# Kernel optimization log

Measured on AMD Instinct MI355X. Metric: run time of the kernel, lower is better.

Reference implementation:

```python
import jax, jax.numpy as jnp
import numpy as np

D_MODEL = 2048; D_STATE = 128; D_CONV = 4; EXPAND = 2
HEADDIM = 64; NGROUPS = 1; CHUNK = 256
D_INNER = EXPAND * D_MODEL          # 4096
NHEADS = D_INNER // HEADDIM         # 64
HG = NHEADS // NGROUPS              # heads per group
CONV_DIM = D_INNER + 2 * NGROUPS * D_STATE          # 4352
D_IN_PROJ = 2 * D_INNER + 2 * NGROUPS * D_STATE + NHEADS  # 8512
BATCH = 2; SEQLEN = 2048
EPS = 1e-5


def setup_inputs() -> dict:
    ks = jax.random.split(jax.random.key(0), 8)
    u = jax.random.normal(ks[0], (BATCH, SEQLEN, D_MODEL), jnp.float32)
    in_proj_w = jax.random.normal(ks[1], (D_IN_PROJ, D_MODEL), jnp.float32) * D_MODEL ** -0.5
    conv_w = jax.random.normal(ks[2], (CONV_DIM, D_CONV), jnp.float32) * D_CONV ** -0.5
    conv_b = jax.random.normal(ks[3], (CONV_DIM,), jnp.float32) * 0.1
    # dt_bias init exactly as in the module: inv softplus of dt ~ U(log(1e-3), log(1e-1))
    dt = jnp.exp(jax.random.uniform(ks[4], (NHEADS,), jnp.float32)
                 * (np.float32(np.log(0.1)) - np.float32(np.log(0.001))) + np.float32(np.log(0.001)))
    dt = jnp.clip(dt, 1e-4, None)
    dt_bias = dt + jnp.log(-jnp.expm1(-dt))
    A_log = jnp.log(jax.random.uniform(ks[5], (NHEADS,), jnp.float32, minval=1.0, maxval=16.0))
    D_skip = jnp.ones((NHEADS,), jnp.float32)
    norm_w = jnp.ones((D_INNER,), jnp.float32)
    out_proj_w = jax.random.normal(ks[6], (D_MODEL, D_INNER), jnp.float32) * D_INNER ** -0.5
    return dict(u=u, in_proj_w=in_proj_w, conv_w=conv_w, conv_b=conv_b,
                dt_bias=dt_bias, A_log=A_log, D_skip=D_skip,
                norm_w=norm_w, out_proj_w=out_proj_w)


def _mamba2(u, in_proj_w, conv_w, conv_b, dt_bias, A_log, D_skip, norm_w, out_proj_w):
    b, l, _ = u.shape
    nc = l // CHUNK
    zxbcdt = u @ in_proj_w.T                                   # (b,l,d_in_proj)
    z = zxbcdt[..., :D_INNER]                                  # gate
    xBC = zxbcdt[..., D_INNER:D_INNER + CONV_DIM]
    dt = jax.nn.softplus(zxbcdt[..., D_INNER + CONV_DIM:] + dt_bias)  # (b,l,h)
    # causal depthwise conv1d (padding d_conv-1, truncated to seqlen) + SiLU
    xp = jnp.pad(xBC, ((0, 0), (D_CONV - 1, 0), (0, 0)))
    conv = conv_b + sum(conv_w[:, k] * xp[:, k:k + l, :] for k in range(D_CONV))
    xBC = jax.nn.silu(conv)
    x = xBC[..., :D_INNER].reshape(b, l, NHEADS, HEADDIM)
    Bm = xBC[..., D_INNER:D_INNER + NGROUPS * D_STATE].reshape(b, l, NGROUPS, D_STATE)
    Cm = xBC[..., D_INNER + NGROUPS * D_STATE:].reshape(b, l, NGROUPS, D_STATE)
    A = -jnp.exp(A_log)                                        # (h,)
    # ---- SSD chunked scan ----
    xc = x.reshape(b, nc, CHUNK, NGROUPS, HG, HEADDIM)         # (b,c,s,g,H,p)
    dtc = dt.reshape(b, nc, CHUNK, NGROUPS, HG)                # (b,c,s,g,H)
    Bc = Bm.reshape(b, nc, CHUNK, NGROUPS, D_STATE)            # (b,c,s,g,n)
    Cc = Cm.reshape(b, nc, CHUNK, NGROUPS, D_STATE)
    dA = jnp.transpose(dtc * A.reshape(NGROUPS, HG), (0, 3, 4, 1, 2))  # (b,g,H,c,s)
    dA_cs = jnp.cumsum(dA, axis=-1)                            # (b,g,H,c,s)
    # intra-chunk: L[i,j] = exp(sum_{j<k<=i} dA_k), lower-triangular (diag=1)
    seg = dA_cs[..., :, None] - dA_cs[..., None, :]            # (b,g,H,c,l,s)
    tri = jnp.tril(jnp.ones((CHUNK, CHUNK), bool))
    Lmat = jnp.where(tri, jnp.exp(seg), 0.0)
    xdt = xc * dtc[..., None]                                  # (b,c,s,g,H,p)
    CB = jnp.einsum('bclgn,bcsgn->bcgls', Cc, Bc)
    Y_diag = jnp.einsum('bcgls,bgHcls,bcsgHp->bclgHp', CB, Lmat, xdt)
    # chunk states and inter-chunk recurrence
    decay_states = jnp.exp(dA_cs[..., -1:] - dA_cs)            # (b,g,H,c,s)
    states = jnp.einsum('bcsgn,bgHcs,bcsgHp->bcgHpn', Bc, decay_states, xdt)
    chunk_decay = jnp.exp(dA_cs[..., -1])                      # (b,g,H,c)

    def step(carry, inp):
        st, dec = inp
        return carry * dec[..., None, None] + st, carry

    _, prev = jax.lax.scan(step, jnp.zeros_like(states[:, 0]),
                           (jnp.moveaxis(states, 1, 0), jnp.moveaxis(chunk_decay, -1, 0)))
    prev = jnp.moveaxis(prev, 0, 1)                            # (b,c,g,H,p,n) state entering chunk
    Y_off = jnp.einsum('bclgn,bcgHpn,bgHcl->bclgHp', Cc, prev, jnp.exp(dA_cs))
    y = (Y_diag + Y_off).reshape(b, l, NHEADS, HEADDIM) + x * D_skip[None, None, :, None]
    y = y.reshape(b, l, D_INNER)
    # gated RMSNorm: gate first (norm_before_gate=False), groupwise rms (ngroups=1 -> full)
    y = y * jax.nn.silu(z)
    yg = y.reshape(b, l, NGROUPS, D_INNER // NGROUPS)
    yg = yg * jax.lax.rsqrt(jnp.mean(yg * yg, axis=-1, keepdims=True) + EPS)
    y = yg.reshape(b, l, D_INNER) * norm_w
    return y @ out_proj_w.T                                    # (b,l,d_model)


def reference(u, in_proj_w, conv_w, conv_b, dt_bias, A_log, D_skip, norm_w, out_proj_w):
    return _mamba2(u, in_proj_w, conv_w, conv_b, dt_bias, A_log, D_skip, norm_w, out_proj_w)
```

## Files before the change

### kernel.cpp

```cpp
#include <hip/hip_runtime.h>
#include <hip/hip_bf16.h>


#define D_MODEL   2048
#define D_STATE   128
#define HEADDIM   64
#define CHUNK     256
#define D_INNER   4096
#define NHEADS    64
#define CONV_DIM  4352
#define D_IN_PROJ 8512
#define SEQLEN    2048
#define NC        8
#define ROWSTOT   4096
#define NPAD      8576
#define RMS_EPS   1e-5f

#define OFF_WIN   0ull
#define OFF_XBF   0ull
#define OFF_PREV  0ull
#define OFF_WOUT  16777216ull
#define OFF_UBF   35127296ull
#define OFF_DTV   35127296ull
#define OFF_DACS  36175872ull
#define OFF_BBF   37224448ull
#define OFF_CBF   38273024ull
#define OFF_CB    39321600ull
#define OFF_BT    43515904ull
#define OFF_XBC   51904512ull
#define OFF_STATE 51904512ull
#define OFF_ZBF   87556096ull
#define OFF_DTRAW 121110528ull
#define OFF_YBUF  121110528ull
#define WS_NEEDED 154664960ull

#define N4_U    2097152l
#define N4_WIN  4390912l

typedef __hip_bfloat16 bf16;
typedef __bf16 bfrag8 __attribute__((ext_vector_type(8)));
typedef float  f32x4v __attribute__((ext_vector_type(4)));

__device__ __forceinline__ f32x4v mfma16(bfrag8 a, bfrag8 b, f32x4v c) {
  return __builtin_amdgcn_mfma_f32_16x16x32_bf16(a, b, c, 0, 0, 0);
}

__device__ __forceinline__ void gload_lds16(const void* g, void* l) {
  __builtin_amdgcn_global_load_lds((const __attribute__((address_space(1))) void*)g,
                                   (__attribute__((address_space(3))) void*)l, 16, 0, 0);
}

__device__ __forceinline__ bf16 f2b(float x) { return __float2bfloat16(x); }
__device__ __forceinline__ float b2f(bf16 x) { return __bfloat162float(x); }
__device__ __forceinline__ float siluf(float x) { return x / (1.f + __expf(-x)); }

__global__ __launch_bounds__(256) void cast_all_kernel(const float* __restrict__ u,
    const float* __restrict__ w_in,
    bf16* __restrict__ u_bf, bf16* __restrict__ win_bf) {
  long i = (long)blockIdx.x * 256 + threadIdx.x;
  if (i < N4_U) {
    float4 v = ((const float4*)u)[i];
    bf16* o = u_bf + i * 4;
    o[0] = f2b(v.x); o[1] = f2b(v.y); o[2] = f2b(v.z); o[3] = f2b(v.w);
  } else if (i < N4_U + N4_WIN) {
    long e = (i - N4_U) * 4;
    long row = e / D_MODEL;
    bf16* o = win_bf + e;
    if (row < D_IN_PROJ) {
      float4 v = *(const float4*)(w_in + e);
      o[0] = f2b(v.x); o[1] = f2b(v.y); o[2] = f2b(v.z); o[3] = f2b(v.w);
    } else {
      bf16 z = f2b(0.f);
      o[0] = z; o[1] = z; o[2] = z; o[3] = z;
    }
  }
}

__global__ __launch_bounds__(256) void cast_kernel(const float* __restrict__ in,
                                                   bf16* __restrict__ out, long n4) {
  long i = (long)blockIdx.x * 256 + threadIdx.x;
  if (i >= n4) return;
  float4 v = ((const float4*)in)[i];
  bf16* o = out + i * 4;
  o[0] = f2b(v.x); o[1] = f2b(v.y); o[2] = f2b(v.z); o[3] = f2b(v.w);
}


__global__ __launch_bounds__(512) void gemm1_kernel(const bf16* __restrict__ A,
                                                    const bf16* __restrict__ B,
                                                    bf16* __restrict__ zb,
                                                    bf16* __restrict__ xbc,
                                                    float* __restrict__ dtraw) {
  int pid = blockIdx.x;
  int t = pid & 63, s = pid >> 6;
  int sm = s / 9, sn = s % 9;
  int xcd = t & 7, j8 = t >> 3;
  int tm = sm * 8 + (xcd >> 1) * 2 + (j8 & 1);
  int tn = sn * 8 + (xcd & 1) * 4 + (j8 >> 1);
  if (tn >= 67) return;
  long row0 = (long)tm * 256, col0 = (long)tn * 128;

  __shared__ __align__(16) bf16 As[2 * 256 * 32];
  __shared__ __align__(16) bf16 Bs[2 * 128 * 32];
  int tid = threadIdx.x, lane = tid & 63, w = tid >> 6;
  int wr = w >> 1, wc = w & 1, r16 = lane & 15, q = lane >> 4;
  int qs = (q ^ ((r16 >> 1) & 3)) * 8;
  const int K = D_MODEL;
  f32x4v zero4 = {0.f, 0.f, 0.f, 0.f};
  f32x4v acc[4][4];
#pragma unroll
  for (int i = 0; i < 4; ++i)
#pragma unroll
    for (int j = 0; j < 4; ++j) acc[i][j] = zero4;

  for (int kt = 0; kt < K; kt += 64) {
    __syncthreads();
#pragma unroll
    for (int j = 0; j < 4; ++j) {
      int ci = j * 512 + tid;
      int half = ci >> 10, cj = ci & 1023;
      int r = cj >> 2;
      int ko = half * 32 + ((cj & 3) ^ ((cj >> 3) & 3)) * 8;
      gload_lds16(A + (row0 + r) * (long)K + kt + ko,
                  (char*)As + j * 8192 + w * 1024);
    }
#pragma unroll
    for (int j = 0; j < 2; ++j) {
      int ci = j * 512 + tid;
      int half = ci >> 9, cj = ci & 511;
      int r = cj >> 2;
      int ko = half * 32 + ((cj & 3) ^ ((cj >> 3) & 3)) * 8;
      gload_lds16(B + (col0 + r) * (long)K + kt + ko,
                  (char*)Bs + j * 8192 + w * 1024);
    }
    __syncthreads();
#pragma unroll
    for (int ks = 0; ks < 2; ++ks) {
      const bf16* Ab = As + ks * 8192;
      const bf16* Bb = Bs + ks * 4096;
      bfrag8 af[4], bfv[4];
#pragma unroll
      for (int i = 0; i < 4; ++i) af[i]  = *(const bfrag8*)(Ab + (wr * 64 + i * 16 + r16) * 32 + qs);
#pragma unroll
      for (int i = 0; i < 4; ++i) bfv[i] = *(const bfrag8*)(Bb + (wc * 64 + i * 16 + r16) * 32 + qs);
#pragma unroll
      for (int i = 0; i < 4; ++i)
#pragma unroll
        for (int j = 0; j < 4; ++j) acc[i][j] = mfma16(af[i], bfv[j], acc[i][j]);
    }
  }
#pragma unroll
  for (int i = 0; i < 4; ++i)
#pragma unroll
    for (int j = 0; j < 4; ++j) {
      long col = col0 + wc * 64 + j * 16 + r16;
#pragma unroll
      for (int r = 0; r < 4; ++r) {
        long row = row0 + wr * 64 + i * 16 + q * 4 + r;
        float v = acc[i][j][r];
        if (col < D_INNER)                       zb[row * D_INNER + col] = f2b(v);
        else if (col < D_INNER + CONV_DIM)       xbc[row * CONV_DIM + (col - D_INNER)] = f2b(v);
        else if (col < D_IN_PROJ)                dtraw[row * NHEADS + (col - D_INNER - CONV_DIM)] = v;
      }
    }
}

__global__ __launch_bounds__(512) void gemm2_kernel(const bf16* __restrict__ A,
                                                    const bf16* __restrict__ B,
                                                    float* __restrict__ C) {
  int pid = blockIdx.x;
  int t = pid & 63, s = pid >> 6;
  int sm = s >> 1, sn = s & 1;
  int xcd = t & 7, j8 = t >> 3;
  int tm = sm * 8 + (xcd >> 1) * 2 + (j8 & 1);
  int tn = sn * 8 + (xcd & 1) * 4 + (j8 >> 1);
  long row0 = (long)tm * 256, col0 = (long)tn * 128;

  __shared__ __align__(16) bf16 As[2 * 256 * 32];
  __shared__ __align__(16) bf16 Bs[2 * 128 * 32];
  int tid = threadIdx.x, lane = tid & 63, w = tid >> 6;
  int wr = w >> 1, wc = w & 1, r16 = lane & 15, q = lane >> 4;
  int qs = (q ^ ((r16 >> 1) & 3)) * 8;
  const int K = D_INNER, ldc = D_MODEL;
  f32x4v zero4 = {0.f, 0.f, 0.f, 0.f};
  f32x4v acc[4][4];
#pragma unroll
  for (int i = 0; i < 4; ++i)
#pragma unroll
    for (int j = 0; j < 4; ++j) acc[i][j] = zero4;

  for (int kt = 0; kt < K; kt += 64) {
    __syncthreads();
#pragma unroll
    for (int j = 0; j < 4; ++j) {
      int ci = j * 512 + tid;
      int half = ci >> 10, cj = ci & 1023;
      int r = cj >> 2;
      int ko = half * 32 + ((cj & 3) ^ ((cj >> 3) & 3)) * 8;
      gload_lds16(A + (row0 + r) * (long)K + kt + ko,
                  (char*)As + j * 8192 + w * 1024);
    }
#pragma unroll
    for (int j = 0; j < 2; ++j) {
      int ci = j * 512 + tid;
      int half = ci >> 9, cj = ci & 511;
      int r = cj >> 2;
      int ko = half * 32 + ((cj & 3) ^ ((cj >> 3) & 3)) * 8;
      gload_lds16(B + (col0 + r) * (long)K + kt + ko,
                  (char*)Bs + j * 8192 + w * 1024);
    }
    __syncthreads();
#pragma unroll
    for (int ks = 0; ks < 2; ++ks) {
      const bf16* Ab = As + ks * 8192;
      const bf16* Bb = Bs + ks * 4096;
      bfrag8 af[4], bfv[4];
#pragma unroll
      for (int i = 0; i < 4; ++i) af[i]  = *(const bfrag8*)(Ab + (wr * 64 + i * 16 + r16) * 32 + qs);
#pragma unroll
      for (int i = 0; i < 4; ++i) bfv[i] = *(const bfrag8*)(Bb + (wc * 64 + i * 16 + r16) * 32 + qs);
#pragma unroll
      for (int i = 0; i < 4; ++i)
#pragma unroll
        for (int j = 0; j < 4; ++j) acc[i][j] = mfma16(af[i], bfv[j], acc[i][j]);
    }
  }
#pragma unroll
  for (int i = 0; i < 4; ++i)
#pragma unroll
    for (int j = 0; j < 4; ++j)
#pragma unroll
      for (int r = 0; r < 4; ++r) {
        long row = row0 + wr * 64 + i * 16 + q * 4 + r;
        long col = col0 + wc * 64 + j * 16 + r16;
        C[row * ldc + col] = acc[i][j][r];
      }
}

__global__ __launch_bounds__(256) void dt_scan_kernel(const float* __restrict__ dtraw,
    const float* __restrict__ dt_bias, const float* __restrict__ A_log,
    float* __restrict__ dtv_buf, float* __restrict__ dacs_buf) {
  int blk = blockIdx.x;
  int c = blk & 7, h = (blk >> 3) & 63, b = blk >> 9;
  int s = threadIdx.x, lane = s & 63, w = s >> 6;
  long row = (long)b * SEQLEN + c * CHUNK + s;
  float raw = dtraw[row * NHEADS + h] + dt_bias[h];
  float dtv = fmaxf(raw, 0.f) + log1pf(__expf(-fabsf(raw)));
  float A = -__expf(A_log[h]);
  float x = dtv * A;
#pragma unroll
  for (int off = 1; off < 64; off <<= 1) {
    float y = __shfl_up(x, off);
    if (lane >= off) x += y;
  }
  __shared__ __align__(16) float wsum[4];
  if (lane == 63) wsum[w] = x;
  __syncthreads();
  float pre = 0.f;
#pragma unroll
  for (int i = 0; i < 4; ++i) pre += (i < w) ? wsum[i] : 0.f;
  long o = ((long)(b * NHEADS + h) * NC + c) * CHUNK + s;
  dtv_buf[o] = dtv;
  dacs_buf[o] = x + pre;
}

__global__ __launch_bounds__(256) void conv_kernel(const bf16* __restrict__ xbc,
    const float* __restrict__ conv_w, const float* __restrict__ conv_b,
    bf16* __restrict__ xo, bf16* __restrict__ Bo, bf16* __restrict__ Co,
    bf16* __restrict__ BT) {
  int cidx = blockIdx.x * 256 + threadIdx.x;
  int l0 = blockIdx.y * 8, b = blockIdx.z;
  float4 wv = *(const float4*)(conv_w + cidx * 4);
  float bias = conv_b[cidx];
  const bf16* base = xbc + (long)b * SEQLEN * CONV_DIM + cidx;
  float win[11];
#pragma unroll
  for (int k = 0; k < 11; ++k) {
    int ls = l0 - 3 + k;
    win[k] = (ls >= 0) ? b2f(base[(long)ls * CONV_DIM]) : 0.f;
  }
  int cgrp = (cidx < D_INNER) ? 0 : ((cidx < D_INNER + D_STATE) ? 1 : 2);
  int n = cidx - D_INNER;
  int n2 = cidx - D_INNER - D_STATE;
  int cch = l0 >> 8;
#pragma unroll
  for (int j = 0; j < 8; ++j) {
    float acc = bias + wv.x * win[j] + wv.y * win[j + 1] + wv.z * win[j + 2] + wv.w * win[j + 3];
    bf16 o = f2b(siluf(acc));
    int l = l0 + j;
    long rowo = (long)b * SEQLEN + l;
    if (cgrp == 0) {
      xo[rowo * D_INNER + cidx] = o;
    } else if (cgrp == 1) {
      Bo[rowo * D_STATE + n] = o;
      BT[(((long)b * NC + cch) * D_STATE + n) * CHUNK + (l & 255)] = o;
    } else {
      Co[rowo * D_STATE + n2] = o;
    }
  }
}

__global__ __launch_bounds__(256) void cb_kernel(const bf16* __restrict__ Cg,
                                                 const bf16* __restrict__ Bg,
                                                 float* __restrict__ CB) {
  int blk = blockIdx.x;
  int stile = blk & 3, bc = blk >> 2;
  int c = bc & 7, b = bc >> 3;
  int tid = threadIdx.x, lane = tid & 63, w = tid >> 6, r16 = lane & 15, q = lane >> 4;
  const bf16* Cb = Cg + ((long)b * SEQLEN + c * CHUNK) * D_STATE;
  const bf16* Bb = Bg + ((long)b * SEQLEN + c * CHUNK) * D_STATE;
  bfrag8 af[4][4];
#pragma unroll
  for (int lt = 0; lt < 4; ++lt)
#pragma unroll
    for (int kk = 0; kk < 4; ++kk)
      af[lt][kk] = *(const bfrag8*)(Cb + (long)(w * 64 + lt * 16 + r16) * D_STATE + kk * 32 + q * 8);
  float* CBb = CB + (long)bc * CHUNK * CHUNK;
  f32x4v zero4 = {0.f, 0.f, 0.f, 0.f};
  for (int st = stile * 4; st < stile * 4 + 4; ++st) {
    f32x4v acc[4] = {zero4, zero4, zero4, zero4};
#pragma unroll
    for (int kk = 0; kk < 4; ++kk) {
      bfrag8 bfv = *(const bfrag8*)(Bb + (long)(st * 16 + r16) * D_STATE + kk * 32 + q * 8);
#pragma unroll
      for (int lt = 0; lt < 4; ++lt) acc[lt] = mfma16(af[lt][kk], bfv, acc[lt]);
    }
#pragma unroll
    for (int lt = 0; lt < 4; ++lt)
#pragma unroll
      for (int r = 0; r < 4; ++r)
        CBb[(long)(w * 64 + lt * 16 + q * 4 + r) * CHUNK + st * 16 + r16] = acc[lt][r];
  }
}

__global__ __launch_bounds__(256) void ssm_diag_kernel(
    const bf16* __restrict__ xg, const bf16* __restrict__ BT,
    const float* __restrict__ CB, const float* __restrict__ dtv_buf,
    const float* __restrict__ dacs_buf, const float* __restrict__ Dskip,
    bf16* __restrict__ ybuf, float* __restrict__ states) {
  int blk = blockIdx.x;
  int h = blk & 63, cc = (blk >> 6) & 7, b = blk >> 9;
  int tid = threadIdx.x, lane = tid & 63, w = tid >> 6, r16 = lane & 15, q = lane >> 4;

  __shared__ __align__(16) __bf16 xT[HEADDIM][264];
  __shared__ __align__(16) float cs_s[CHUNK];
  __shared__ __align__(16) float dt_s[CHUNK];
  __shared__ __align__(16) float w_s[CHUNK];

  long hco = ((long)(b * NHEADS + h) * NC + cc) * CHUNK;
  cs_s[tid] = dacs_buf[hco + tid];
  dt_s[tid] = dtv_buf[hco + tid];
  __syncthreads();
  float cl_last = cs_s[CHUNK - 1];
  w_s[tid] = __expf(cl_last - cs_s[tid]) * dt_s[tid];

  const __bf16* xbase = (const __bf16*)(xg + ((long)b * SEQLEN + cc * CHUNK) * D_INNER + h * HEADDIM);
#pragma unroll
  for (int it = 0; it < 8; ++it) {
    int e = it * 256 + tid;
    int s = e >> 3, p0 = (e & 7) * 8;
    bfrag8 xv = *(const bfrag8*)(xbase + (long)s * D_INNER + p0);
#pragma unroll
    for (int j = 0; j < 8; ++j) xT[p0 + j][s] = xv[j];
  }
  __syncthreads();

  const float* CBchunk = CB + (long)(b * NC + cc) * CHUNK * CHUNK;
  const __bf16* BTc = (const __bf16*)(BT + (((long)b * NC + cc) * D_STATE) * CHUNK);
  f32x4v zero4 = {0.f, 0.f, 0.f, 0.f};
  f32x4v accY[4][4], accS[2][4];
#pragma unroll
  for (int i = 0; i < 4; ++i)
#pragma unroll
    for (int j = 0; j < 4; ++j) accY[i][j] = zero4;
#pragma unroll
  for (int i = 0; i < 2; ++i)
#pragma unroll
    for (int j = 0; j < 4; ++j) accS[i][j] = zero4;

  int l_row[4];
  const float* CBrow[4];
#pragma unroll
  for (int lt = 0; lt < 4; ++lt) {
    l_row[lt] = w * 64 + lt * 16 + r16;
    CBrow[lt] = CBchunk + (long)l_row[lt] * CHUNK;
  }

#pragma unroll 2
  for (int ks = 0; ks < 8; ++ks) {
    int s0 = ks * 32 + q * 8;
    float4 cs0 = *(const float4*)(cs_s + s0);
    float4 cs1 = *(const float4*)(cs_s + s0 + 4);
    float4 dt0 = *(const float4*)(dt_s + s0);
    float4 dt1 = *(const float4*)(dt_s + s0 + 4);
    float4 w0  = *(const float4*)(w_s + s0);
    float4 w1  = *(const float4*)(w_s + s0 + 4);
    float csv[8] = {cs0.x, cs0.y, cs0.z, cs0.w, cs1.x, cs1.y, cs1.z, cs1.w};
    float dtv8[8] = {dt0.x, dt0.y, dt0.z, dt0.w, dt1.x, dt1.y, dt1.z, dt1.w};
    float wv8[8]  = {w0.x, w0.y, w0.z, w0.w, w1.x, w1.y, w1.z, w1.w};

    bfrag8 xf[4];
#pragma unroll
    for (int pt = 0; pt < 4; ++pt) xf[pt] = *(const bfrag8*)(&xT[pt * 16 + r16][s0]);

#pragma unroll
    for (int lt = 0; lt < 4; ++lt) {
      int l = l_row[lt];
      float cs_l = cs_s[l];
      float4 cb0 = *(const float4*)(CBrow[lt] + s0);
      float4 cb1 = *(const float4*)(CBrow[lt] + s0 + 4);
      float cbv[8] = {cb0.x, cb0.y, cb0.z, cb0.w, cb1.x, cb1.y, cb1.z, cb1.w};
      bfrag8 pf;
#pragma unroll
      for (int j = 0; j < 8; ++j) {
        float v = (s0 + j <= l)
                    ? cbv[j] * __expf(fminf(cs_l - csv[j], 0.f)) * dtv8[j]
                    : 0.f;
        pf[j] = (__bf16)v;
      }
#pragma unroll
      for (int pt = 0; pt < 4; ++pt) accY[lt][pt] = mfma16(pf, xf[pt], accY[lt][pt]);
    }

#pragma unroll
    for (int nt = 0; nt < 2; ++nt) {
      int n = w * 32 + nt * 16 + r16;
      bfrag8 braw = *(const bfrag8*)(BTc + (long)n * CHUNK + s0);
      bfrag8 bwf;
#pragma unroll
      for (int j = 0; j < 8; ++j) bwf[j] = (__bf16)((float)braw[j] * wv8[j]);
#pragma unroll
      for (int pt = 0; pt < 4; ++pt) accS[nt][pt] = mfma16(bwf, xf[pt], accS[nt][pt]);
    }
  }

  float dsk = Dskip[h];
  bf16* ybase = ybuf + ((long)b * SEQLEN + cc * CHUNK) * D_INNER + h * HEADDIM;
#pragma unroll
  for (int lt = 0; lt < 4; ++lt)
#pragma unroll
    for (int pt = 0; pt < 4; ++pt)
#pragma unroll
      for (int r = 0; r < 4; ++r) {
        int lrow = w * 64 + lt * 16 + q * 4 + r;
        int pcol = pt * 16 + r16;
        ybase[(long)lrow * D_INNER + pcol] = f2b(accY[lt][pt][r] + (float)xT[pcol][lrow] * dsk);
      }
  float* sbase = states + (long)blk * (HEADDIM * D_STATE);
#pragma unroll
  for (int nt = 0; nt < 2; ++nt)
#pragma unroll
    for (int pt = 0; pt < 4; ++pt)
#pragma unroll
      for (int r = 0; r < 4; ++r)
        sbase[(long)(pt * 16 + r16) * D_STATE + w * 32 + nt * 16 + q * 4 + r] = accS[nt][pt][r];
}

__global__ __launch_bounds__(256) void state_scan_kernel(const float* __restrict__ states,
    const float* __restrict__ dacs, bf16* __restrict__ prevb) {
  int gid = blockIdx.x;
  int et = gid & 31, bh = gid >> 5;
  int h = bh & 63, b = bh >> 6;
  int e = et * 256 + threadIdx.x;
  float dec[NC];
#pragma unroll
  for (int c = 0; c < NC; ++c)
    dec[c] = __expf(dacs[((long)(b * NHEADS + h) * NC + c) * CHUNK + (CHUNK - 1)]);
  float carry = 0.f;
#pragma unroll
  for (int c = 0; c < NC; ++c) {
    long off = ((long)((b * NC + c) * NHEADS + h)) * (HEADDIM * D_STATE) + e;
    prevb[off] = f2b(carry);
    carry = carry * dec[c] + states[off];
  }
}

__global__ __launch_bounds__(256) void yoff_kernel(const bf16* __restrict__ Cg,
    const bf16* __restrict__ prevb, const float* __restrict__ dacs,
    bf16* __restrict__ ybuf) {
  int blk = blockIdx.x;
  int h = blk & 63, cc = (blk >> 6) & 7, b = blk >> 9;
  int tid = threadIdx.x, lane = tid & 63, w = tid >> 6, r16 = lane & 15, q = lane >> 4;
  __shared__ __align__(16) float cs_s[CHUNK];
  cs_s[tid] = dacs[((long)(b * NHEADS + h) * NC + cc) * CHUNK + tid];
  __syncthreads();
  const bf16* Cb = Cg + ((long)b * SEQLEN + cc * CHUNK) * D_STATE;
  const bf16* Pb = prevb + (long)blk * (HEADDIM * D_STATE);
  f32x4v zero4 = {0.f, 0.f, 0.f, 0.f};
  f32x4v acc[4][4];
#pragma unroll
  for (int i = 0; i < 4; ++i)
#pragma unroll
    for (int j = 0; j < 4; ++j) acc[i][j] = zero4;
#pragma unroll
  for (int kk = 0; kk < 4; ++kk) {
    bfrag8 bv[4];
#pragma unroll
    for (int pt = 0; pt < 4; ++pt)
      bv[pt] = *(const bfrag8*)(Pb + (long)(pt * 16 + r16) * D_STATE + kk * 32 + q * 8);
#pragma unroll
    for (int lt = 0; lt < 4; ++lt) {
      bfrag8 av = *(const bfrag8*)(Cb + (long)(w * 64 + lt * 16 + r16) * D_STATE + kk * 32 + q * 8);
#pragma unroll
      for (int pt = 0; pt < 4; ++pt) acc[lt][pt] = mfma16(av, bv[pt], acc[lt][pt]);
    }
  }
  bf16* ybase = ybuf + ((long)b * SEQLEN + cc * CHUNK) * D_INNER + h * HEADDIM;
#pragma unroll
  for (int lt = 0; lt < 4; ++lt)
#pragma unroll
    for (int pt = 0; pt < 4; ++pt)
#pragma unroll
      for (int r = 0; r < 4; ++r) {
        int lrow = w * 64 + lt * 16 + q * 4 + r;
        float ef = __expf(cs_s[lrow]);
        bf16* p = ybase + (long)lrow * D_INNER + pt * 16 + r16;
        *p = f2b(b2f(*p) + acc[lt][pt][r] * ef);
      }
}

__global__ __launch_bounds__(256) void gate_norm_kernel(bf16* __restrict__ ybuf,
    const bf16* __restrict__ zb, const float* __restrict__ norm_w) {
  int row = blockIdx.x, tid = threadIdx.x;
  bf16* y = ybuf + (long)row * D_INNER;
  const bf16* z = zb + (long)row * D_INNER;
  float v[16];
  float ss = 0.f;
#pragma unroll
  for (int i = 0; i < 2; ++i) {
    int e = tid * 16 + i * 8;
    bfrag8 yv = *(const bfrag8*)(y + e);
    bfrag8 zv = *(const bfrag8*)(z + e);
#pragma unroll
    for (int j = 0; j < 8; ++j) {
      float a = (float)yv[j] * siluf((float)zv[j]);
      v[i * 8 + j] = a;
      ss += a * a;
    }
  }
#pragma unroll
  for (int off = 32; off > 0; off >>= 1) ss += __shfl_down(ss, off);
  __shared__ __align__(16) float red[4];
  int lane = tid & 63, w = tid >> 6;
  if (lane == 0) red[w] = ss;
  __syncthreads();
  float tot = red[0] + red[1] + red[2] + red[3];
  float scale = rsqrtf(tot * (1.f / D_INNER) + RMS_EPS);
#pragma unroll
  for (int i = 0; i < 2; ++i) {
    int e = tid * 16 + i * 8;
    float4 w0 = *(const float4*)(norm_w + e);
    float4 w1 = *(const float4*)(norm_w + e + 4);
    bfrag8 o;
    o[0] = (__bf16)(v[i * 8 + 0] * scale * w0.x);
    o[1] = (__bf16)(v[i * 8 + 1] * scale * w0.y);
    o[2] = (__bf16)(v[i * 8 + 2] * scale * w0.z);
    o[3] = (__bf16)(v[i * 8 + 3] * scale * w0.w);
    o[4] = (__bf16)(v[i * 8 + 4] * scale * w1.x);
    o[5] = (__bf16)(v[i * 8 + 5] * scale * w1.y);
    o[6] = (__bf16)(v[i * 8 + 6] * scale * w1.z);
    o[7] = (__bf16)(v[i * 8 + 7] * scale * w1.w);
    *(bfrag8*)(y + e) = o;
  }
}

extern "C" void kernel_launch(void* const* d_in, const int* in_sizes, int n_in,
                              void* d_out, int out_size, void* d_ws, size_t ws_size,
                              hipStream_t stream) {
  if (ws_size < WS_NEEDED) return;

  const float* u       = (const float*)d_in[0];
  const float* w_in    = (const float*)d_in[1];
  const float* conv_w  = (const float*)d_in[2];
  const float* conv_b  = (const float*)d_in[3];
  const float* dt_bias = (const float*)d_in[4];
  const float* A_log   = (const float*)d_in[5];
  const float* Dskip   = (const float*)d_in[6];
  const float* norm_w  = (const float*)d_in[7];
  const float* w_out   = (const float*)d_in[8];
  float* out = (float*)d_out;

  char* ws = (char*)d_ws;
  bf16*  win_bf  = (bf16*)(ws + OFF_WIN);
  bf16*  x_bf    = (bf16*)(ws + OFF_XBF);
  bf16*  prevb   = (bf16*)(ws + OFF_PREV);
  bf16*  wout_bf = (bf16*)(ws + OFF_WOUT);
  bf16*  u_bf    = (bf16*)(ws + OFF_UBF);
  float* dtv     = (float*)(ws + OFF_DTV);
  float* dacs    = (float*)(ws + OFF_DACS);
  bf16*  B_bf    = (bf16*)(ws + OFF_BBF);
  bf16*  C_bf    = (bf16*)(ws + OFF_CBF);
  float* CBb     = (float*)(ws + OFF_CB);
  bf16*  BT_bf   = (bf16*)(ws + OFF_BT);
  bf16*  xbc_bf  = (bf16*)(ws + OFF_XBC);
  float* states  = (float*)(ws + OFF_STATE);
  bf16*  z_bf    = (bf16*)(ws + OFF_ZBF);
  float* dt_raw  = (float*)(ws + OFF_DTRAW);
  bf16*  ybuf    = (bf16*)(ws + OFF_YBUF);

  cast_all_kernel<<<25344, 256, 0, stream>>>(u, w_in, u_bf, win_bf);
  gemm1_kernel<<<1152, 512, 0, stream>>>(u_bf, win_bf, z_bf, xbc_bf, dt_raw);
  dt_scan_kernel<<<1024, 256, 0, stream>>>(dt_raw, dt_bias, A_log, dtv, dacs);
  conv_kernel<<<dim3(17, SEQLEN / 8, 2), 256, 0, stream>>>(xbc_bf, conv_w, conv_b, x_bf, B_bf, C_bf, BT_bf);
  cb_kernel<<<64, 256, 0, stream>>>(C_bf, B_bf, CBb);
  ssm_diag_kernel<<<1024, 256, 0, stream>>>(x_bf, BT_bf, CBb, dtv, dacs, Dskip, ybuf, states);
  state_scan_kernel<<<4096, 256, 0, stream>>>(states, dacs, prevb);
  yoff_kernel<<<1024, 256, 0, stream>>>(C_bf, prevb, dacs, ybuf);
  cast_kernel<<<8192, 256, 0, stream>>>(w_out, wout_bf, (long)D_MODEL * D_INNER / 4);
  gate_norm_kernel<<<ROWSTOT, 256, 0, stream>>>(ybuf, z_bf, norm_w);
  gemm2_kernel<<<256, 512, 0, stream>>>(ybuf, wout_bf, out);
}
```

Baseline: 597.6 us.

## Merge independent small kernels and shrink gemm2 tiles to raise block count

Fuses dt_scan with the conv kernel, and the w_out cast with gate-norm, into single launches that branch on block index. This removes launch gaps and lets the independent work share the GPU. gemm2 moves from 256x128 tiles with 512 threads to 128x128 tiles with 256 threads, doubling the grid to 512 blocks for better CU coverage across 256 CUs. In exchange, smaller tiles reuse each loaded operand across fewer outputs.

Result: faster. 562.6 us (-5.9%).

```diff
diff --git a/kernel.cpp b/kernel.cpp
--- a/kernel.cpp
+++ b/kernel.cpp
@@ -76,15 +76,6 @@
   }
 }
 
-__global__ __launch_bounds__(256) void cast_kernel(const float* __restrict__ in,
-                                                   bf16* __restrict__ out, long n4) {
-  long i = (long)blockIdx.x * 256 + threadIdx.x;
-  if (i >= n4) return;
-  float4 v = ((const float4*)in)[i];
-  bf16* o = out + i * 4;
-  o[0] = f2b(v.x); o[1] = f2b(v.y); o[2] = f2b(v.z); o[3] = f2b(v.w);
-}
-
 
 __global__ __launch_bounds__(512) void gemm1_kernel(const bf16* __restrict__ A,
                                                     const bf16* __restrict__ B,
@@ -165,7 +156,7 @@
     }
 }
 
-__global__ __launch_bounds__(512) void gemm2_kernel(const bf16* __restrict__ A,
+__global__ __launch_bounds__(256) void gemm2_kernel(const bf16* __restrict__ A,
                                                     const bf16* __restrict__ B,
                                                     float* __restrict__ C) {
   int pid = blockIdx.x;
@@ -174,9 +165,9 @@
   int xcd = t & 7, j8 = t >> 3;
   int tm = sm * 8 + (xcd >> 1) * 2 + (j8 & 1);
   int tn = sn * 8 + (xcd & 1) * 4 + (j8 >> 1);
-  long row0 = (long)tm * 256, col0 = (long)tn * 128;
-
-  __shared__ __align__(16) bf16 As[2 * 256 * 32];
+  long row0 = (long)tm * 128, col0 = (long)tn * 128;
+
+  __shared__ __align__(16) bf16 As[2 * 128 * 32];
   __shared__ __align__(16) bf16 Bs[2 * 128 * 32];
   int tid = threadIdx.x, lane = tid & 63, w = tid >> 6;
   int wr = w >> 1, wc = w & 1, r16 = lane & 15, q = lane >> 4;
@@ -193,26 +184,26 @@
     __syncthreads();
 #pragma unroll
     for (int j = 0; j < 4; ++j) {
-      int ci = j * 512 + tid;
-      int half = ci >> 10, cj = ci & 1023;
+      int ci = (j * 4 + w) * 64 + lane;
+      int half = ci >> 9, cj = ci & 511;
       int r = cj >> 2;
       int ko = half * 32 + ((cj & 3) ^ ((cj >> 3) & 3)) * 8;
       gload_lds16(A + (row0 + r) * (long)K + kt + ko,
-                  (char*)As + j * 8192 + w * 1024);
-    }
-#pragma unroll
-    for (int j = 0; j < 2; ++j) {
-      int ci = j * 512 + tid;
+                  (char*)As + (j * 4 + w) * 1024);
+    }
+#pragma unroll
+    for (int j = 0; j < 4; ++j) {
+      int ci = (j * 4 + w) * 64 + lane;
       int half = ci >> 9, cj = ci & 511;
       int r = cj >> 2;
       int ko = half * 32 + ((cj & 3) ^ ((cj >> 3) & 3)) * 8;
       gload_lds16(B + (col0 + r) * (long)K + kt + ko,
-                  (char*)Bs + j * 8192 + w * 1024);
+                  (char*)Bs + (j * 4 + w) * 1024);
     }
     __syncthreads();
 #pragma unroll
     for (int ks = 0; ks < 2; ++ks) {
-      const bf16* Ab = As + ks * 8192;
+      const bf16* Ab = As + ks * 4096;
       const bf16* Bb = Bs + ks * 4096;
       bfrag8 af[4], bfv[4];
 #pragma unroll
@@ -237,39 +228,44 @@
       }
 }
 
-__global__ __launch_bounds__(256) void dt_scan_kernel(const float* __restrict__ dtraw,
-    const float* __restrict__ dt_bias, const float* __restrict__ A_log,
-    float* __restrict__ dtv_buf, float* __restrict__ dacs_buf) {
-  int blk = blockIdx.x;
-  int c = blk & 7, h = (blk >> 3) & 63, b = blk >> 9;
-  int s = threadIdx.x, lane = s & 63, w = s >> 6;
-  long row = (long)b * SEQLEN + c * CHUNK + s;
-  float raw = dtraw[row * NHEADS + h] + dt_bias[h];
-  float dtv = fmaxf(raw, 0.f) + log1pf(__expf(-fabsf(raw)));
-  float A = -__expf(A_log[h]);
-  float x = dtv * A;
-#pragma unroll
-  for (int off = 1; off < 64; off <<= 1) {
-    float y = __shfl_up(x, off);
-    if (lane >= off) x += y;
-  }
-  __shared__ __align__(16) float wsum[4];
-  if (lane == 63) wsum[w] = x;
-  __syncthreads();
-  float pre = 0.f;
-#pragma unroll
-  for (int i = 0; i < 4; ++i) pre += (i < w) ? wsum[i] : 0.f;
-  long o = ((long)(b * NHEADS + h) * NC + c) * CHUNK + s;
-  dtv_buf[o] = dtv;
-  dacs_buf[o] = x + pre;
-}
-
-__global__ __launch_bounds__(256) void conv_kernel(const bf16* __restrict__ xbc,
-    const float* __restrict__ conv_w, const float* __restrict__ conv_b,
-    bf16* __restrict__ xo, bf16* __restrict__ Bo, bf16* __restrict__ Co,
-    bf16* __restrict__ BT) {
-  int cidx = blockIdx.x * 256 + threadIdx.x;
-  int l0 = blockIdx.y * 8, b = blockIdx.z;
+__global__ __launch_bounds__(256) void conv_dt_kernel(
+    const float* __restrict__ dtraw, const float* __restrict__ dt_bias,
+    const float* __restrict__ A_log, float* __restrict__ dtv_buf,
+    float* __restrict__ dacs_buf,
+    const bf16* __restrict__ xbc, const float* __restrict__ conv_w,
+    const float* __restrict__ conv_b, bf16* __restrict__ xo,
+    bf16* __restrict__ Bo, bf16* __restrict__ Co, bf16* __restrict__ BT) {
+  if (blockIdx.x < 1024) {
+    int blk = blockIdx.x;
+    int c = blk & 7, h = (blk >> 3) & 63, b = blk >> 9;
+    int s = threadIdx.x, lane = s & 63, w = s >> 6;
+    long row = (long)b * SEQLEN + c * CHUNK + s;
+    float raw = dtraw[row * NHEADS + h] + dt_bias[h];
+    float dtv = fmaxf(raw, 0.f) + log1pf(__expf(-fabsf(raw)));
+    float A = -__expf(A_log[h]);
+    float x = dtv * A;
+#pragma unroll
+    for (int off = 1; off < 64; off <<= 1) {
+      float y = __shfl_up(x, off);
+      if (lane >= off) x += y;
+    }
+    __shared__ __align__(16) float wsum[4];
+    if (lane == 63) wsum[w] = x;
+    __syncthreads();
+    float pre = 0.f;
+#pragma unroll
+    for (int i = 0; i < 4; ++i) pre += (i < w) ? wsum[i] : 0.f;
+    long o = ((long)(b * NHEADS + h) * NC + c) * CHUNK + s;
+    dtv_buf[o] = dtv;
+    dacs_buf[o] = x + pre;
+    return;
+  }
+  int t = blockIdx.x - 1024;
+  int bx = t % 17;
+  int rest = t / 17;
+  int by = rest & 255, bz = rest >> 8;
+  int cidx = bx * 256 + threadIdx.x;
+  int l0 = by * 8, b = bz;
   float4 wv = *(const float4*)(conv_w + cidx * 4);
   float bias = conv_b[cidx];
   const bf16* base = xbc + (long)b * SEQLEN * CONV_DIM + cidx;
@@ -519,9 +515,18 @@
       }
 }
 
-__global__ __launch_bounds__(256) void gate_norm_kernel(bf16* __restrict__ ybuf,
-    const bf16* __restrict__ zb, const float* __restrict__ norm_w) {
-  int row = blockIdx.x, tid = threadIdx.x;
+__global__ __launch_bounds__(256) void cast_gate_kernel(
+    const float* __restrict__ w_out, bf16* __restrict__ wout_bf,
+    bf16* __restrict__ ybuf, const bf16* __restrict__ zb,
+    const float* __restrict__ norm_w) {
+  if (blockIdx.x < 8192) {
+    long i = (long)blockIdx.x * 256 + threadIdx.x;
+    float4 v = ((const float4*)w_out)[i];
+    bf16* o = wout_bf + i * 4;
+    o[0] = f2b(v.x); o[1] = f2b(v.y); o[2] = f2b(v.z); o[3] = f2b(v.w);
+    return;
+  }
+  int row = blockIdx.x - 8192, tid = threadIdx.x;
   bf16* y = ybuf + (long)row * D_INNER;
   const bf16* z = zb + (long)row * D_INNER;
   float v[16];
@@ -600,13 +605,12 @@
 
   cast_all_kernel<<<25344, 256, 0, stream>>>(u, w_in, u_bf, win_bf);
   gemm1_kernel<<<1152, 512, 0, stream>>>(u_bf, win_bf, z_bf, xbc_bf, dt_raw);
-  dt_scan_kernel<<<1024, 256, 0, stream>>>(dt_raw, dt_bias, A_log, dtv, dacs);
-  conv_kernel<<<dim3(17, SEQLEN / 8, 2), 256, 0, stream>>>(xbc_bf, conv_w, conv_b, x_bf, B_bf, C_bf, BT_bf);
+  conv_dt_kernel<<<9728, 256, 0, stream>>>(dt_raw, dt_bias, A_log, dtv, dacs,
+                                           xbc_bf, conv_w, conv_b, x_bf, B_bf, C_bf, BT_bf);
   cb_kernel<<<64, 256, 0, stream>>>(C_bf, B_bf, CBb);
   ssm_diag_kernel<<<1024, 256, 0, stream>>>(x_bf, BT_bf, CBb, dtv, dacs, Dskip, ybuf, states);
   state_scan_kernel<<<4096, 256, 0, stream>>>(states, dacs, prevb);
   yoff_kernel<<<1024, 256, 0, stream>>>(C_bf, prevb, dacs, ybuf);
-  cast_kernel<<<8192, 256, 0, stream>>>(w_out, wout_bf, (long)D_MODEL * D_INNER / 4);
-  gate_norm_kernel<<<ROWSTOT, 256, 0, stream>>>(ybuf, z_bf, norm_w);
-  gemm2_kernel<<<256, 512, 0, stream>>>(ybuf, wout_bf, out);
-}
+  cast_gate_kernel<<<12288, 256, 0, stream>>>(w_out, wout_bf, ybuf, z_bf, norm_w);
+  gemm2_kernel<<<512, 256, 0, stream>>>(ybuf, wout_bf, out);
+}
```
